# Kernel tuning notes

Hardware: AMD Instinct MI355X
Metric: run time of the kernel (lower is better)

## Reference

```python
import jax, jax.numpy as jnp
import numpy as np

T, B, OBS, H, P, L, A = 512, 128, 512, 256, 128, 4, 4


def _ln(x, scale, bias, eps=1e-6):
    mu = jnp.mean(x, axis=-1, keepdims=True)
    var = jnp.mean((x - mu) ** 2, axis=-1, keepdims=True)
    return (x - mu) * jax.lax.rsqrt(var + eps) * scale + bias


def _binop(qi, qj):
    # S5 reset-aware associative operator: elements (A, b, reset_flag)
    Ai, bi, ci = qi
    Aj, bj, cj = qj
    A = (Aj * Ai) * (1.0 - cj) + Aj * cj
    b = (Aj * bi + bj) * (1.0 - cj) + bj * cj
    c = ci * (1.0 - cj) + cj
    return A, b, c


def _s5_layer(x, dones, h0, scale, bias, lam_re, lam_im, b_re, b_im, c_re, c_im, d_vec, log_step, glu_W, glu_b):
    # x: (T,B,H) real, dones: (T,B), h0: (B,P) complex64
    skip = x
    u = _ln(x, scale, bias)                                  # prenorm
    lam = lam_re + 1j * lam_im                               # (P,)
    step = jnp.exp(log_step)                                 # (P,)
    lam_bar = jnp.exp(lam * step)                            # ZOH discretization
    B_bar = ((lam_bar - 1.0) / lam)[:, None] * (b_re + 1j * b_im)  # (P,H)
    Bu = jnp.einsum('tbh,ph->tbp', u.astype(jnp.complex64), B_bar)  # (T,B,P)
    A_el = jnp.concatenate([jnp.ones((1, B, P), jnp.complex64),
                            jnp.broadcast_to(lam_bar.astype(jnp.complex64), (T, B, P))], axis=0)
    b_el = jnp.concatenate([h0[None], Bu], axis=0)
    c_el = jnp.concatenate([jnp.zeros((1, B, 1), jnp.float32), dones[..., None]], axis=0)
    _, xs, _ = jax.lax.associative_scan(_binop, (A_el, b_el, c_el), axis=0)
    xs = xs[1:]                                              # (T,B,P) complex states
    new_h = xs[-1]
    C = c_re + 1j * c_im                                     # (H,P)
    ys = 2.0 * jnp.real(jnp.einsum('tbp,hp->tbh', xs, C)) + d_vec * u  # conj_sym output + D*u
    z = _ln(ys, scale, bias)                                 # gtrxl norm (shared LayerNorm params)
    z = jax.nn.gelu(z)                                       # half_glu1
    z = z * jax.nn.sigmoid(z @ glu_W + glu_b)
    return skip + z, new_h


def setup_inputs() -> dict:
    key = jax.random.key(0)
    ks = jax.random.split(key, 40)
    f32 = jnp.float32

    def n(i, shape, s=1.0):
        return jax.random.normal(ks[i], shape, f32) * s

    inp = {}
    inp['obs'] = n(0, (T, B, OBS))
    inp['dones'] = (jax.random.uniform(ks[1], (T, B)) < 0.01).astype(f32)
    inp['hidden_re'] = jnp.zeros((L, B, P), f32)
    inp['hidden_im'] = jnp.zeros((L, B, P), f32)
    inp['enc0_W'] = n(2, (OBS, 128), 1.0 / np.sqrt(OBS))
    inp['enc0_b'] = jnp.zeros((128,), f32)
    inp['enc1_W'] = n(3, (128, H), 1.0 / np.sqrt(128))
    inp['enc1_b'] = jnp.zeros((H,), f32)
    inp['norm_scale'] = jnp.ones((L, H), f32)
    inp['norm_bias'] = jnp.zeros((L, H), f32)
    inp['Lambda_re'] = -0.5 * jax.random.uniform(ks[4], (L, P), f32) - 0.1
    inp['Lambda_im'] = n(5, (L, P), np.pi)
    inp['B_re'] = n(6, (L, P, H), 1.0 / np.sqrt(H))
    inp['B_im'] = n(7, (L, P, H), 1.0 / np.sqrt(H))
    inp['C_re'] = n(8, (L, H, P), 1.0 / np.sqrt(2 * P))
    inp['C_im'] = n(9, (L, H, P), 1.0 / np.sqrt(2 * P))
    inp['D'] = n(10, (L, H))
    inp['log_step'] = jax.random.uniform(ks[11], (L, P), f32, np.log(1e-3), np.log(1e-1))
    inp['glu_W'] = n(12, (L, H, H), 1.0 / np.sqrt(H))
    inp['glu_b'] = jnp.zeros((L, H), f32)
    inp['ab0_W'] = n(13, (H, 128), 1.0 / np.sqrt(H))
    inp['ab0_b'] = jnp.zeros((128,), f32)
    inp['ab1_W'] = n(14, (128, 128), 1.0 / np.sqrt(128))
    inp['ab1_b'] = jnp.zeros((128,), f32)
    inp['adec_W'] = n(15, (128, A), 0.01 / np.sqrt(128))
    inp['adec_b'] = jnp.full((A,), 0.5, f32)
    inp['log_std'] = jnp.full((A,), -0.7, f32)
    inp['vb0_W'] = n(16, (H, 128), 1.0 / np.sqrt(H))
    inp['vb0_b'] = jnp.zeros((128,), f32)
    inp['vb1_W'] = n(17, (128, 128), 1.0 / np.sqrt(128))
    inp['vb1_b'] = jnp.zeros((128,), f32)
    inp['vdec_W'] = n(18, (128, 1), 1.0 / np.sqrt(128))
    inp['vdec_b'] = jnp.zeros((1,), f32)
    return inp


def reference(obs, dones, hidden_re, hidden_im, enc0_W, enc0_b, enc1_W, enc1_b,
              norm_scale, norm_bias, Lambda_re, Lambda_im, B_re, B_im, C_re, C_im,
              D, log_step, glu_W, glu_b, ab0_W, ab0_b, ab1_W, ab1_b, adec_W, adec_b,
              log_std, vb0_W, vb0_b, vb1_W, vb1_b, vdec_W, vdec_b):
    e = jax.nn.leaky_relu(obs @ enc0_W + enc0_b)
    e = jax.nn.leaky_relu(e @ enc1_W + enc1_b)
    h0 = (hidden_re + 1j * hidden_im).astype(jnp.complex64)  # (L,B,P)
    new_h = []
    for l in range(L):
        e, hl = _s5_layer(e, dones, h0[l], norm_scale[l], norm_bias[l],
                          Lambda_re[l], Lambda_im[l], B_re[l], B_im[l],
                          C_re[l], C_im[l], D[l], log_step[l], glu_W[l], glu_b[l])
        new_h.append(hl)
    new_h = jnp.stack(new_h)
    am = jax.nn.leaky_relu(e @ ab0_W + ab0_b)
    am = jax.nn.leaky_relu(am @ ab1_W + ab1_b)
    am = am @ adec_W + adec_b                                # actor mean (T,B,A)
    v = jax.nn.leaky_relu(e @ vb0_W + vb0_b)
    v = jax.nn.leaky_relu(v @ vb1_W + vb1_b)
    v = v @ vdec_W + vdec_b                                  # critic (T,B,1)
    sc = jnp.broadcast_to(jnp.exp(log_std), am.shape)        # Normal scale (pi params)
    out = jnp.concatenate([am, sc, v], axis=-1)              # (T,B,2A+1)
    return out, jnp.real(new_h), jnp.imag(new_h)
```

## Files before the change

kernel.cpp:

```cpp
#include <hip/hip_runtime.h>
#include <math.h>

#define TT 512
#define BB 128
#define OBSD 512
#define HD 256
#define PD 128
#define LD 4
#define NTB (TT*BB)

typedef __bf16 bf16x8 __attribute__((ext_vector_type(8)));
typedef float  f32x4  __attribute__((ext_vector_type(4)));

__device__ __forceinline__ float bf2f(unsigned short u) {
    return __uint_as_float(((unsigned)u) << 16);
}
__device__ __forceinline__ unsigned short f2bf(float f) {
    unsigned u = __float_as_uint(f);
    unsigned r = (u + 0x7FFFu + ((u >> 16) & 1u)) >> 16;
    return (unsigned short)r;
}
__device__ __forceinline__ float gelu_f(float x) {
    float x3 = x * x * x;
    return 0.5f * x * (1.f + tanhf(0.7978845608028654f * (x + 0.044715f * x3)));
}

template<int MODE, int NJ>
__global__ __launch_bounds__(512) void mgemm2(
    const unsigned short* __restrict__ A, const unsigned short* __restrict__ BT,
    int K, int LDA, const float* __restrict__ bias,
    const float* __restrict__ lnsc, const float* __restrict__ lnbi,
    const unsigned short* __restrict__ aux1, unsigned short* Xio,
    unsigned short* __restrict__ U, int wU)
{
    constexpr int NJW = NJ / 2;
    constexpr int LPS = 2 + NJW;
    const int N = NJ * 64;
    __shared__ unsigned short smA[3 * 2048];
    __shared__ unsigned short smB[3 * NJ * 2048];
    float2 (*red)[8] = reinterpret_cast<float2(*)[8]>(&smA[0]);
    int tid = threadIdx.x;
    int lane = tid & 63, w = tid >> 6;
    int m16 = lane & 15, quad = lane >> 4;
    int m0 = blockIdx.x * 64;

    f32x4 acc[4][NJW] = {};

    auto stage = [&](int slot, int kt) {
        int k0 = kt << 5;
#pragma unroll
        for (int j = 0; j < 2; ++j) {
            int chunk = w * 2 + j;
            int e = chunk * 128 + lane * 2;
            int row = e >> 5, kb = e & 31;
            const unsigned short* g = A + (size_t)(m0 + row) * LDA + k0 + kb;
            __builtin_amdgcn_global_load_lds(
                (const __attribute__((address_space(1))) void*)g,
                (__attribute__((address_space(3))) void*)(smA + slot * 2048 + chunk * 128 + lane * 2),
                4, 0, 0);
        }
#pragma unroll
        for (int j = 0; j < NJW; ++j) {
            int chunk = w * NJW + j;
            int e = chunk * 512 + lane * 8;
            int p = e >> 11, r = (e >> 5) & 63, kq = e & 31;
            const unsigned short* g = BT + (size_t)(p * 64 + r) * K + k0 + kq;
            __builtin_amdgcn_global_load_lds(
                (const __attribute__((address_space(1))) void*)g,
                (__attribute__((address_space(3))) void*)(smB + slot * NJ * 2048 + chunk * 512 + lane * 8),
                16, 0, 0);
        }
    };

    int nk = K >> 5;
    stage(0, 0);
    stage(1, 1);
    int cur = 0, nxt = 2;
    for (int t = 0; t < nk; ++t) {
        int rem = nk - 1 - t;
        if (rem >= 2) {
            stage(nxt, t + 2);
            nxt = (nxt == 2) ? 0 : nxt + 1;
            asm volatile("s_waitcnt vmcnt(%0)" :: "i"(2 * LPS) : "memory");
        } else if (rem == 1) {
            asm volatile("s_waitcnt vmcnt(%0)" :: "i"(LPS) : "memory");
        } else {
            asm volatile("s_waitcnt vmcnt(0)" ::: "memory");
        }
        __builtin_amdgcn_s_barrier();
        __builtin_amdgcn_sched_barrier(0);
        bf16x8 af[4], bfr[NJW];
#pragma unroll
        for (int mi = 0; mi < 4; ++mi)
            af[mi] = *(const bf16x8*)(smA + cur * 2048 + (mi * 16 + m16) * 32 + quad * 8);
#pragma unroll
        for (int nj = 0; nj < NJW; ++nj)
            bfr[nj] = *(const bf16x8*)(smB + cur * NJ * 2048 + (w * NJW + nj) * 512 + m16 * 32 + quad * 8);
#pragma unroll
        for (int mi = 0; mi < 4; ++mi)
#pragma unroll
            for (int nj = 0; nj < NJW; ++nj)
                acc[mi][nj] = __builtin_amdgcn_mfma_f32_16x16x32_bf16(
                    bfr[nj], af[mi], acc[mi][nj], 0, 0, 0);
        __builtin_amdgcn_sched_barrier(0);
        __builtin_amdgcn_s_barrier();
        cur = (cur == 2) ? 0 : cur + 1;
    }

    int colb = w * (NJW * 16) + quad * 4;

    if (MODE == 1) {
#pragma unroll
        for (int mi = 0; mi < 4; ++mi) {
            size_t rowb = (size_t)(m0 + mi * 16 + m16) * N;
#pragma unroll
            for (int nj = 0; nj < NJW; ++nj) {
                ushort4 o = { f2bf(acc[mi][nj][0]), f2bf(acc[mi][nj][1]),
                              f2bf(acc[mi][nj][2]), f2bf(acc[mi][nj][3]) };
                *(ushort4*)(U + rowb + colb + nj * 16) = o;
            }
        }
        return;
    }

#pragma unroll
    for (int mi = 0; mi < 4; ++mi) {
        size_t rowb = (size_t)(m0 + mi * 16 + m16) * N;
        float s = 0.f, q = 0.f;
#pragma unroll
        for (int nj = 0; nj < NJW; ++nj) {
            float4 bn = *(const float4*)(bias + colb + nj * 16);
            ushort4 a1, xo;
            if (MODE == 2 || MODE == 3) a1 = *(const ushort4*)(aux1 + rowb + colb + nj * 16);
            if (MODE == 3)              xo = *(const ushort4*)(Xio + rowb + colb + nj * 16);
            float vv[4];
#pragma unroll
            for (int r = 0; r < 4; ++r) {
                float v = acc[mi][nj][r];
                float bv = (r == 0) ? bn.x : (r == 1) ? bn.y : (r == 2) ? bn.z : bn.w;
                if (MODE == 0 || MODE == 4) {
                    v += bv; v = v > 0.f ? v : 0.01f * v;
                } else if (MODE == 2) {
                    float u = bf2f(r == 0 ? a1.x : r == 1 ? a1.y : r == 2 ? a1.z : a1.w);
                    v += bv * u;
                } else if (MODE == 3) {
                    float zz = bf2f(r == 0 ? a1.x : r == 1 ? a1.y : r == 2 ? a1.z : a1.w);
                    float xx = bf2f(r == 0 ? xo.x : r == 1 ? xo.y : r == 2 ? xo.z : xo.w);
                    float sg = 1.f / (1.f + expf(-(v + bv)));
                    v = xx + zz * sg;
                }
                vv[r] = v;
                acc[mi][nj][r] = v;
                s += v; q += v * v;
            }
            if (MODE == 0 || MODE == 3) {
                ushort4 o = { f2bf(vv[0]), f2bf(vv[1]), f2bf(vv[2]), f2bf(vv[3]) };
                *(ushort4*)(Xio + rowb + colb + nj * 16) = o;
            } else if (MODE == 4) {
                ushort4 o = { f2bf(vv[0]), f2bf(vv[1]), f2bf(vv[2]), f2bf(vv[3]) };
                *(ushort4*)(U + rowb + colb + nj * 16) = o;
            }
        }
        if (MODE != 4 && (MODE != 3 || wU)) {
            s += __shfl_xor(s, 16); q += __shfl_xor(q, 16);
            s += __shfl_xor(s, 32); q += __shfl_xor(q, 32);
            if (quad == 0) red[mi * 16 + m16][w] = float2{s, q};
        }
    }
    if (MODE == 4 || (MODE == 3 && !wU)) return;
    __syncthreads();

#pragma unroll
    for (int mi = 0; mi < 4; ++mi) {
        int row_l = mi * 16 + m16;
        float S = 0.f, Q = 0.f;
#pragma unroll
        for (int ww = 0; ww < 8; ++ww) {
            float2 tv = red[row_l][ww];
            S += tv.x; Q += tv.y;
        }
        float mu = S * (1.f / 256.f);
        float var = Q * (1.f / 256.f) - mu * mu;
        float rstd = rsqrtf(var + 1e-6f);
        size_t rowb = (size_t)(m0 + row_l) * N;
#pragma unroll
        for (int nj = 0; nj < NJW; ++nj) {
            float4 ls = *(const float4*)(lnsc + colb + nj * 16);
            float4 lb = *(const float4*)(lnbi + colb + nj * 16);
            float o[4];
#pragma unroll
            for (int r = 0; r < 4; ++r) {
                float sc = (r == 0) ? ls.x : (r == 1) ? ls.y : (r == 2) ? ls.z : ls.w;
                float bi = (r == 0) ? lb.x : (r == 1) ? lb.y : (r == 2) ? lb.z : lb.w;
                float v = (acc[mi][nj][r] - mu) * rstd * sc + bi;
                if (MODE == 2) v = gelu_f(v);
                o[r] = v;
            }
            ushort4 ov = { f2bf(o[0]), f2bf(o[1]), f2bf(o[2]), f2bf(o[3]) };
            *(ushort4*)(U + rowb + colb + nj * 16) = ov;
        }
    }
}

__global__ __launch_bounds__(256) void mgemm_obs(
    const float* __restrict__ A, const unsigned short* __restrict__ BT,
    unsigned short* __restrict__ U, const float* __restrict__ bias)
{
    const int K = 512, NJ = 2, N = 128;
    __shared__ unsigned short smA[64 * 32];
    __shared__ unsigned short smB[NJ * 64 * 32];
    int tid = threadIdx.x;
    int lane = tid & 63, w = tid >> 6;
    int m16 = lane & 15, quad = lane >> 4;
    int m0 = blockIdx.x * 64;

    f32x4 acc[4][NJ] = {};
    for (int k0 = 0; k0 < K; k0 += 32) {
#pragma unroll
        for (int p = 0; p < 2; ++p) {
            int idx = p * 256 + tid;
            int r = idx >> 3, kq = (idx & 7) * 4;
            float4 v = *(const float4*)(A + (size_t)(m0 + r) * K + k0 + kq);
            ushort4 o = { f2bf(v.x), f2bf(v.y), f2bf(v.z), f2bf(v.w) };
            *(ushort4*)(smA + r * 32 + kq) = o;
        }
#pragma unroll
        for (int p = 0; p < NJ; ++p) {
            const unsigned short* g = BT + (size_t)(p * 64 + (tid >> 2)) * K + k0 + (tid & 3) * 8;
            unsigned short* l = smB + p * 2048 + tid * 8;
            __builtin_amdgcn_global_load_lds(
                (const __attribute__((address_space(1))) void*)g,
                (__attribute__((address_space(3))) void*)l, 16, 0, 0);
        }
        __syncthreads();
        bf16x8 af[4], bfr[NJ];
#pragma unroll
        for (int mi = 0; mi < 4; ++mi)
            af[mi] = *(const bf16x8*)(smA + (mi * 16 + m16) * 32 + quad * 8);
#pragma unroll
        for (int nj = 0; nj < NJ; ++nj)
            bfr[nj] = *(const bf16x8*)(smB + (w * NJ * 16 + nj * 16 + m16) * 32 + quad * 8);
#pragma unroll
        for (int mi = 0; mi < 4; ++mi)
#pragma unroll
            for (int nj = 0; nj < NJ; ++nj)
                acc[mi][nj] = __builtin_amdgcn_mfma_f32_16x16x32_bf16(
                    bfr[nj], af[mi], acc[mi][nj], 0, 0, 0);
        __syncthreads();
    }
    int colb = w * NJ * 16 + quad * 4;
#pragma unroll
    for (int mi = 0; mi < 4; ++mi) {
        size_t rowb = (size_t)(m0 + mi * 16 + m16) * N;
#pragma unroll
        for (int nj = 0; nj < NJ; ++nj) {
            float4 bv = *(const float4*)(bias + colb + nj * 16);
            float v0 = acc[mi][nj][0] + bv.x; v0 = v0 > 0.f ? v0 : 0.01f * v0;
            float v1 = acc[mi][nj][1] + bv.y; v1 = v1 > 0.f ? v1 : 0.01f * v1;
            float v2 = acc[mi][nj][2] + bv.z; v2 = v2 > 0.f ? v2 : 0.01f * v2;
            float v3 = acc[mi][nj][3] + bv.w; v3 = v3 > 0.f ? v3 : 0.01f * v3;
            ushort4 o = { f2bf(v0), f2bf(v1), f2bf(v2), f2bf(v3) };
            *(ushort4*)(U + rowb + colb + nj * 16) = o;
        }
    }
}

__global__ __launch_bounds__(512) void scan2_k(
    const unsigned short* __restrict__ bu, unsigned short* __restrict__ xs,
    const float* __restrict__ dones,
    const float* __restrict__ h0re, const float* __restrict__ h0im,
    const float* __restrict__ lamre, const float* __restrict__ lamim,
    const float* __restrict__ lstep,
    float* __restrict__ outre, float* __restrict__ outim)
{
    __shared__ float sdone[TT];
    __shared__ float4 ssum[8][64];
    __shared__ float2 shin[8][64];
    int tid = threadIdx.x;
    int b  = blockIdx.x >> 1;
    int ph = blockIdx.x & 1;
    int chunk = tid >> 6, pl = tid & 63;
    int p = ph * 64 + pl;
    sdone[tid] = dones[tid * BB + b];
    float lr = lamre[p], li = lamim[p];
    float st = expf(lstep[p]);
    float er = expf(lr * st);
    float ar = er * cosf(li * st);
    float ai = er * sinf(li * st);
    __syncthreads();

    int t0 = chunk * 64;
    unsigned buf[64];
    float Ar = 1.f, Ai = 0.f, br = 0.f, bi = 0.f;
#pragma unroll
    for (int j = 0; j < 64; ++j) {
        size_t off = ((size_t)(t0 + j) * BB + b) * 256 + 2 * p;
        unsigned v = *(const unsigned*)(bu + off);
        buf[j] = v;
        float bur = bf2f((unsigned short)(v & 0xFFFFu));
        float bui = bf2f((unsigned short)(v >> 16));
        if (sdone[t0 + j] != 0.f) {
            Ar = 0.f; Ai = 0.f; br = bur; bi = bui;
        } else {
            float nAr = ar * Ar - ai * Ai;
            float nAi = ar * Ai + ai * Ar;
            float nbr = fmaf(ar, br, fmaf(-ai, bi, bur));
            float nbi = fmaf(ar, bi, fmaf(ai, br, bui));
            Ar = nAr; Ai = nAi; br = nbr; bi = nbi;
        }
    }
    ssum[chunk][pl] = float4{Ar, Ai, br, bi};
    __syncthreads();
    if (tid < 64) {
        int gid = b * 128 + p;
        float hr = h0re[gid], hi = h0im[gid];
#pragma unroll
        for (int c = 0; c < 8; ++c) {
            shin[c][pl] = float2{hr, hi};
            float4 s = ssum[c][pl];
            float nhr = fmaf(s.x, hr, fmaf(-s.y, hi, s.z));
            float nhi = fmaf(s.x, hi, fmaf(s.y, hr, s.w));
            hr = nhr; hi = nhi;
        }
        outre[gid] = hr; outim[gid] = hi;
    }
    __syncthreads();
    float hr = shin[chunk][pl].x, hi = shin[chunk][pl].y;
#pragma unroll
    for (int j = 0; j < 64; ++j) {
        unsigned v = buf[j];
        float bur = bf2f((unsigned short)(v & 0xFFFFu));
        float bui = bf2f((unsigned short)(v >> 16));
        float nr, ni;
        if (sdone[t0 + j] != 0.f) { nr = bur; ni = bui; }
        else {
            nr = fmaf(ar, hr, fmaf(-ai, hi, bur));
            ni = fmaf(ar, hi, fmaf(ai, hr, bui));
        }
        hr = nr; hi = ni;
        size_t off = ((size_t)(t0 + j) * BB + b) * 256 + 2 * p;
        *(unsigned*)(xs + off) = ((unsigned)f2bf(ni) << 16) | f2bf(nr);
    }
}

__global__ __launch_bounds__(256) void prep_k(
    const float* __restrict__ Br, const float* __restrict__ Bi,
    const float* __restrict__ Cr, const float* __restrict__ Ci,
    const float* __restrict__ Lr, const float* __restrict__ Li,
    const float* __restrict__ ls, unsigned short* bbarT, unsigned short* ccatT)
{
    int gid = blockIdx.x * 256 + threadIdx.x;
    int l = gid >> 15;
    int rem = gid & 32767;
    int p = rem >> 8;
    int h = rem & 255;
    float lr = Lr[l * PD + p], li = Li[l * PD + p];
    float st = expf(ls[l * PD + p]);
    float er = expf(lr * st);
    float lbr = er * cosf(li * st);
    float lbi = er * sinf(li * st);
    float nr = lbr - 1.f, ni = lbi;
    float den = lr * lr + li * li;
    float fr = (nr * lr + ni * li) / den;
    float fi = (ni * lr - nr * li) / den;
    float bre = Br[(size_t)(l * PD + p) * HD + h];
    float bim = Bi[(size_t)(l * PD + p) * HD + h];
    size_t lb = (size_t)l * 65536;
    bbarT[lb + (size_t)(2 * p) * 256 + h]     = f2bf(fr * bre - fi * bim);
    bbarT[lb + (size_t)(2 * p + 1) * 256 + h] = f2bf(fr * bim + fi * bre);
    float cre = Cr[(size_t)(l * HD + h) * PD + p];
    float cim = Ci[(size_t)(l * HD + h) * PD + p];
    ccatT[lb + (size_t)h * 256 + 2 * p]     = f2bf(2.f * cre);
    ccatT[lb + (size_t)h * 256 + 2 * p + 1] = f2bf(-2.f * cim);
}

__global__ __launch_bounds__(256) void tcvt_k(const float* __restrict__ in,
    unsigned short* __restrict__ out, int K, int N)
{
    int gid = blockIdx.x * 256 + threadIdx.x;
    if (gid >= K * N) return;
    int k = gid / N, n = gid - k * N;
    out[(size_t)n * K + k] = f2bf(in[gid]);
}

__global__ __launch_bounds__(256) void tcvt4_k(const float* __restrict__ in,
    unsigned short* __restrict__ out)
{
    int gid = blockIdx.x * 256 + threadIdx.x;
    int l = gid >> 16;
    int rem = gid & 65535;
    int k = rem >> 8, n = rem & 255;
    out[(size_t)l * 65536 + (size_t)n * 256 + k] = f2bf(in[gid]);
}

__global__ __launch_bounds__(256) void catb_k(const float* __restrict__ a,
    const float* __restrict__ b, float* __restrict__ out)
{
    int i = threadIdx.x;
    out[i] = (i < 128) ? a[i] : b[i - 128];
}

__global__ __launch_bounds__(256) void head_k(
    const unsigned short* __restrict__ am2, const unsigned short* __restrict__ v2,
    const float* __restrict__ adW, const float* __restrict__ adb,
    const float* __restrict__ lstd,
    const float* __restrict__ vdW, const float* __restrict__ vdb,
    float* out)
{
    int wid = threadIdx.x >> 6, lane = threadIdx.x & 63;
    size_t row = (size_t)blockIdx.x * 4 + wid;
    float a1 = bf2f(am2[row * 128 + lane]);
    float a2 = bf2f(am2[row * 128 + 64 + lane]);
    float w1 = bf2f(v2[row * 128 + lane]);
    float w2 = bf2f(v2[row * 128 + 64 + lane]);
    float vals[5];
#pragma unroll
    for (int a = 0; a < 4; ++a)
        vals[a] = a1 * adW[lane * 4 + a] + a2 * adW[(lane + 64) * 4 + a];
    vals[4] = w1 * vdW[lane] + w2 * vdW[64 + lane];
#pragma unroll
    for (int off = 32; off; off >>= 1)
#pragma unroll
        for (int k = 0; k < 5; ++k) vals[k] += __shfl_xor(vals[k], off);
    if (lane == 0) {
        size_t o = row * 9;
#pragma unroll
        for (int a = 0; a < 4; ++a) out[o + a] = vals[a] + adb[a];
#pragma unroll
        for (int a = 0; a < 4; ++a) out[o + 4 + a] = expf(lstd[a]);
        out[o + 8] = vals[4] + vdb[0];
    }
}

extern "C" void kernel_launch(void* const* d_in, const int* in_sizes, int n_in,
                              void* d_out, int out_size, void* d_ws, size_t ws_size,
                              hipStream_t stream) {
    (void)in_sizes; (void)n_in; (void)out_size; (void)ws_size;
    const float* obs     = (const float*)d_in[0];
    const float* dones   = (const float*)d_in[1];
    const float* hre     = (const float*)d_in[2];
    const float* him     = (const float*)d_in[3];
    const float* enc0_W  = (const float*)d_in[4];
    const float* enc0_b  = (const float*)d_in[5];
    const float* enc1_W  = (const float*)d_in[6];
    const float* enc1_b  = (const float*)d_in[7];
    const float* nsc     = (const float*)d_in[8];
    const float* nbi     = (const float*)d_in[9];
    const float* Lre     = (const float*)d_in[10];
    const float* Lim     = (const float*)d_in[11];
    const float* B_re    = (const float*)d_in[12];
    const float* B_im    = (const float*)d_in[13];
    const float* C_re    = (const float*)d_in[14];
    const float* C_im    = (const float*)d_in[15];
    const float* Dv      = (const float*)d_in[16];
    const float* lstep   = (const float*)d_in[17];
    const float* glu_W   = (const float*)d_in[18];
    const float* glu_b   = (const float*)d_in[19];
    const float* ab0_W   = (const float*)d_in[20];
    const float* ab0_b   = (const float*)d_in[21];
    const float* ab1_W   = (const float*)d_in[22];
    const float* ab1_b   = (const float*)d_in[23];
    const float* adec_W  = (const float*)d_in[24];
    const float* adec_b  = (const float*)d_in[25];
    const float* log_std = (const float*)d_in[26];
    const float* vb0_W   = (const float*)d_in[27];
    const float* vb0_b   = (const float*)d_in[28];
    const float* vb1_W   = (const float*)d_in[29];
    const float* vb1_b   = (const float*)d_in[30];
    const float* vdec_W  = (const float*)d_in[31];
    const float* vdec_b  = (const float*)d_in[32];

    const size_t MB = (size_t)1 << 20;
    char* wsb = (char*)d_ws;
    unsigned short* XS    = (unsigned short*)(wsb);
    unsigned short* AMV1  = (unsigned short*)(wsb);
    unsigned short* AM2   = (unsigned short*)(wsb + 32 * MB);
    unsigned short* V2    = (unsigned short*)(wsb + 48 * MB);
    unsigned short* U1    = (unsigned short*)(wsb + 64 * MB);
    unsigned short* X     = (unsigned short*)(wsb + 96 * MB);
    unsigned short* U     = (unsigned short*)(wsb + 128 * MB);
    unsigned short* BU    = (unsigned short*)(wsb + 160 * MB);
    char* wgt = wsb + 192 * MB;
    unsigned short* BBART = (unsigned short*)(wgt);
    unsigned short* CCATT = (unsigned short*)(wgt + 512 * 1024);
    unsigned short* GLUT  = (unsigned short*)(wgt + 1024 * 1024);
    unsigned short* E0T   = (unsigned short*)(wgt + 1536 * 1024);
    unsigned short* E1T   = (unsigned short*)(wgt + 1664 * 1024);
    unsigned short* AB0VT = (unsigned short*)(wgt + 1728 * 1024);
    unsigned short* AB1T  = (unsigned short*)(wgt + 1856 * 1024);
    unsigned short* VB1T  = (unsigned short*)(wgt + 1888 * 1024);
    float*          CB0   = (float*)(wgt + 1920 * 1024);

    float* out   = (float*)d_out;
    float* outre = out + (size_t)NTB * 9;
    float* outim = outre + LD * BB * PD;

    prep_k<<<512, 256, 0, stream>>>(B_re, B_im, C_re, C_im, Lre, Lim, lstep, BBART, CCATT);
    tcvt_k<<<256, 256, 0, stream>>>(enc0_W, E0T, 512, 128);
    tcvt_k<<<128, 256, 0, stream>>>(enc1_W, E1T, 128, 256);
    tcvt4_k<<<1024, 256, 0, stream>>>(glu_W, GLUT);
    tcvt_k<<<128, 256, 0, stream>>>(ab0_W, AB0VT, 256, 128);
    tcvt_k<<<128, 256, 0, stream>>>(vb0_W, AB0VT + 128 * 256, 256, 128);
    tcvt_k<<<64, 256, 0, stream>>>(ab1_W, AB1T, 128, 128);
    tcvt_k<<<64, 256, 0, stream>>>(vb1_W, VB1T, 128, 128);
    catb_k<<<1, 256, 0, stream>>>(ab0_b, vb0_b, CB0);

    mgemm_obs<<<1024, 256, 0, stream>>>(obs, E0T, U1, enc0_b);
    mgemm2<0, 4><<<1024, 512, 0, stream>>>(U1, E1T, 128, 128, enc1_b, nsc, nbi, nullptr, X, U, 1);

    for (int l = 0; l < LD; ++l) {
        mgemm2<1, 4><<<1024, 512, 0, stream>>>(U, BBART + (size_t)l * 65536, 256, 256,
                                               nullptr, nullptr, nullptr, nullptr, nullptr, BU, 0);
        scan2_k<<<256, 512, 0, stream>>>(BU, XS, dones, hre + l * BB * PD, him + l * BB * PD,
                                         Lre + l * PD, Lim + l * PD, lstep + l * PD,
                                         outre + l * BB * PD, outim + l * BB * PD);
        mgemm2<2, 4><<<1024, 512, 0, stream>>>(XS, CCATT + (size_t)l * 65536, 256, 256,
                                               Dv + l * HD, nsc + l * HD, nbi + l * HD, U, nullptr, U, 1);
        const float* nsc2 = nsc + ((l + 1 < LD) ? (l + 1) * HD : 0);
        const float* nbi2 = nbi + ((l + 1 < LD) ? (l + 1) * HD : 0);
        mgemm2<3, 4><<<1024, 512, 0, stream>>>(U, GLUT + (size_t)l * 65536, 256, 256,
                                               glu_b + l * HD, nsc2, nbi2, U, X, U, (l + 1 < LD) ? 1 : 0);
    }

    mgemm2<4, 4><<<1024, 512, 0, stream>>>(X, AB0VT, 256, 256, CB0, nullptr, nullptr, nullptr, nullptr, AMV1, 0);
    mgemm2<4, 2><<<1024, 512, 0, stream>>>(AMV1, AB1T, 128, 256, ab1_b, nullptr, nullptr, nullptr, nullptr, AM2, 0);
    mgemm2<4, 2><<<1024, 512, 0, stream>>>(AMV1 + 128, VB1T, 128, 256, vb1_b, nullptr, nullptr, nullptr, nullptr, V2, 0);
    head_k<<<NTB / 4, 256, 0, stream>>>(AM2, V2, adec_W, adec_b, log_std, vdec_W, vdec_b, out);
}
```

Before: 960.5 us.

## Fuse GLU with next-layer B projection and fuse MLP heads into one kernel

Adds glu_bu_k, which runs the GLU GEMM, residual and next-layer LayerNorm, then keeps the normalized row tile in shared memory and runs the next layer's B_bar projection without a round trip through global memory. Adds head_fused_k, which chains the actor and critic MLP layers and the decoder dot products in one kernel, replacing three GEMMs and head_k. It also makes K a compile-time template parameter and splits the scan into four P-groups per batch with 16 time chunks to raise parallelism. The cost is more shared memory per block, which may lower occupancy, and the fused kernels use double buffering where the old GEMM used three stages.

```diff
diff --git a/kernel.cpp b/kernel.cpp
--- a/kernel.cpp
+++ b/kernel.cpp
@@ -25,16 +25,17 @@
     return 0.5f * x * (1.f + tanhf(0.7978845608028654f * (x + 0.044715f * x3)));
 }
 
-template<int MODE, int NJ>
+template<int MODE, int NJ, int NK>
 __global__ __launch_bounds__(512) void mgemm2(
     const unsigned short* __restrict__ A, const unsigned short* __restrict__ BT,
-    int K, int LDA, const float* __restrict__ bias,
+    int LDA, const float* __restrict__ bias,
     const float* __restrict__ lnsc, const float* __restrict__ lnbi,
     const unsigned short* __restrict__ aux1, unsigned short* Xio,
     unsigned short* __restrict__ U, int wU)
 {
     constexpr int NJW = NJ / 2;
     constexpr int LPS = 2 + NJW;
+    constexpr int K = NK * 32;
     const int N = NJ * 64;
     __shared__ unsigned short smA[3 * 2048];
     __shared__ unsigned short smB[3 * NJ * 2048];
@@ -56,8 +57,7 @@
             const unsigned short* g = A + (size_t)(m0 + row) * LDA + k0 + kb;
             __builtin_amdgcn_global_load_lds(
                 (const __attribute__((address_space(1))) void*)g,
-                (__attribute__((address_space(3))) void*)(smA + slot * 2048 + chunk * 128 + lane * 2),
-                4, 0, 0);
+                (__attribute__((address_space(3))) void*)(smA + slot * 2048 + e), 4, 0, 0);
         }
 #pragma unroll
         for (int j = 0; j < NJW; ++j) {
@@ -67,12 +67,11 @@
             const unsigned short* g = BT + (size_t)(p * 64 + r) * K + k0 + kq;
             __builtin_amdgcn_global_load_lds(
                 (const __attribute__((address_space(1))) void*)g,
-                (__attribute__((address_space(3))) void*)(smB + slot * NJ * 2048 + chunk * 512 + lane * 8),
-                16, 0, 0);
+                (__attribute__((address_space(3))) void*)(smB + slot * NJ * 2048 + e), 16, 0, 0);
         }
     };
 
-    int nk = K >> 5;
+    int nk = NK;
     stage(0, 0);
     stage(1, 1);
     int cur = 0, nxt = 2;
@@ -138,7 +137,7 @@
             for (int r = 0; r < 4; ++r) {
                 float v = acc[mi][nj][r];
                 float bv = (r == 0) ? bn.x : (r == 1) ? bn.y : (r == 2) ? bn.z : bn.w;
-                if (MODE == 0 || MODE == 4) {
+                if (MODE == 0) {
                     v += bv; v = v > 0.f ? v : 0.01f * v;
                 } else if (MODE == 2) {
                     float u = bf2f(r == 0 ? a1.x : r == 1 ? a1.y : r == 2 ? a1.z : a1.w);
@@ -156,18 +155,15 @@
             if (MODE == 0 || MODE == 3) {
                 ushort4 o = { f2bf(vv[0]), f2bf(vv[1]), f2bf(vv[2]), f2bf(vv[3]) };
                 *(ushort4*)(Xio + rowb + colb + nj * 16) = o;
-            } else if (MODE == 4) {
-                ushort4 o = { f2bf(vv[0]), f2bf(vv[1]), f2bf(vv[2]), f2bf(vv[3]) };
-                *(ushort4*)(U + rowb + colb + nj * 16) = o;
             }
         }
-        if (MODE != 4 && (MODE != 3 || wU)) {
+        if (MODE != 3 || wU) {
             s += __shfl_xor(s, 16); q += __shfl_xor(q, 16);
             s += __shfl_xor(s, 32); q += __shfl_xor(q, 32);
             if (quad == 0) red[mi * 16 + m16][w] = float2{s, q};
         }
     }
-    if (MODE == 4 || (MODE == 3 && !wU)) return;
+    if (MODE == 3 && !wU) return;
     __syncthreads();
 
 #pragma unroll
@@ -199,6 +195,377 @@
             ushort4 ov = { f2bf(o[0]), f2bf(o[1]), f2bf(o[2]), f2bf(o[3]) };
             *(ushort4*)(U + rowb + colb + nj * 16) = ov;
         }
+    }
+}
+
+__global__ __launch_bounds__(512) void glu_bu_k(
+    const unsigned short* __restrict__ Z,
+    const unsigned short* __restrict__ GT,
+    const unsigned short* __restrict__ BT2,
+    const float* __restrict__ glub,
+    const float* __restrict__ ns2, const float* __restrict__ nb2,
+    unsigned short* __restrict__ Xio,
+    unsigned short* __restrict__ Uo,
+    unsigned short* __restrict__ BUo)
+{
+    const int N = 256;
+    __shared__ unsigned short smA[2 * 2048];
+    __shared__ unsigned short smB[2 * 8192];
+    __shared__ unsigned short zbuf[64 * 264];
+    float2 (*red)[8] = reinterpret_cast<float2(*)[8]>(&smA[0]);
+    int tid = threadIdx.x;
+    int lane = tid & 63, w = tid >> 6;
+    int m16 = lane & 15, quad = lane >> 4;
+    int m0 = blockIdx.x * 64;
+    int colb = w * 32 + quad * 4;
+
+    f32x4 acc[4][2] = {};
+
+    auto stage1 = [&](int slot, int kt) {
+        int k0 = kt << 5;
+#pragma unroll
+        for (int j = 0; j < 2; ++j) {
+            int e = (w * 2 + j) * 128 + lane * 2;
+            int row = e >> 5, kb = e & 31;
+            const unsigned short* g = Z + (size_t)(m0 + row) * 256 + k0 + kb;
+            __builtin_amdgcn_global_load_lds(
+                (const __attribute__((address_space(1))) void*)g,
+                (__attribute__((address_space(3))) void*)(smA + slot * 2048 + e), 4, 0, 0);
+        }
+#pragma unroll
+        for (int j = 0; j < 2; ++j) {
+            int e = (w * 2 + j) * 512 + lane * 8;
+            int p = e >> 11, r = (e >> 5) & 63, kq = e & 31;
+            const unsigned short* g = GT + (size_t)(p * 64 + r) * 256 + k0 + kq;
+            __builtin_amdgcn_global_load_lds(
+                (const __attribute__((address_space(1))) void*)g,
+                (__attribute__((address_space(3))) void*)(smB + slot * 8192 + e), 16, 0, 0);
+        }
+    };
+    auto stage2 = [&](int slot, int kt) {
+        int k0 = kt << 5;
+#pragma unroll
+        for (int j = 0; j < 2; ++j) {
+            int e = (w * 2 + j) * 512 + lane * 8;
+            int p = e >> 11, r = (e >> 5) & 63, kq = e & 31;
+            const unsigned short* g = BT2 + (size_t)(p * 64 + r) * 256 + k0 + kq;
+            __builtin_amdgcn_global_load_lds(
+                (const __attribute__((address_space(1))) void*)g,
+                (__attribute__((address_space(3))) void*)(smB + slot * 8192 + e), 16, 0, 0);
+        }
+    };
+
+    stage1(0, 0);
+    for (int t = 0; t < 8; ++t) {
+        int cur = t & 1;
+        if (t + 1 < 8) {
+            stage1(cur ^ 1, t + 1);
+            asm volatile("s_waitcnt vmcnt(4)" ::: "memory");
+        } else {
+            asm volatile("s_waitcnt vmcnt(0)" ::: "memory");
+        }
+        __builtin_amdgcn_s_barrier();
+        __builtin_amdgcn_sched_barrier(0);
+        bf16x8 af[4], bfr[2];
+#pragma unroll
+        for (int mi = 0; mi < 4; ++mi)
+            af[mi] = *(const bf16x8*)(smA + cur * 2048 + (mi * 16 + m16) * 32 + quad * 8);
+#pragma unroll
+        for (int nj = 0; nj < 2; ++nj)
+            bfr[nj] = *(const bf16x8*)(smB + cur * 8192 + (w * 2 + nj) * 512 + m16 * 32 + quad * 8);
+#pragma unroll
+        for (int mi = 0; mi < 4; ++mi)
+#pragma unroll
+            for (int nj = 0; nj < 2; ++nj)
+                acc[mi][nj] = __builtin_amdgcn_mfma_f32_16x16x32_bf16(
+                    bfr[nj], af[mi], acc[mi][nj], 0, 0, 0);
+        __builtin_amdgcn_sched_barrier(0);
+        __builtin_amdgcn_s_barrier();
+    }
+
+    stage2(0, 0);
+
+#pragma unroll
+    for (int mi = 0; mi < 4; ++mi) {
+        int row_l = mi * 16 + m16;
+        size_t rowb = (size_t)(m0 + row_l) * N;
+        float s = 0.f, q = 0.f;
+#pragma unroll
+        for (int nj = 0; nj < 2; ++nj) {
+            float4 gb = *(const float4*)(glub + colb + nj * 16);
+            ushort4 a1 = *(const ushort4*)(Z + rowb + colb + nj * 16);
+            ushort4 xo = *(const ushort4*)(Xio + rowb + colb + nj * 16);
+            float vv[4];
+#pragma unroll
+            for (int r = 0; r < 4; ++r) {
+                float v = acc[mi][nj][r];
+                float bv = (r == 0) ? gb.x : (r == 1) ? gb.y : (r == 2) ? gb.z : gb.w;
+                float zz = bf2f(r == 0 ? a1.x : r == 1 ? a1.y : r == 2 ? a1.z : a1.w);
+                float xx = bf2f(r == 0 ? xo.x : r == 1 ? xo.y : r == 2 ? xo.z : xo.w);
+                float sg = 1.f / (1.f + expf(-(v + bv)));
+                v = xx + zz * sg;
+                vv[r] = v;
+                acc[mi][nj][r] = v;
+                s += v; q += v * v;
+            }
+            ushort4 o = { f2bf(vv[0]), f2bf(vv[1]), f2bf(vv[2]), f2bf(vv[3]) };
+            *(ushort4*)(Xio + rowb + colb + nj * 16) = o;
+        }
+        s += __shfl_xor(s, 16); q += __shfl_xor(q, 16);
+        s += __shfl_xor(s, 32); q += __shfl_xor(q, 32);
+        if (quad == 0) red[row_l][w] = float2{s, q};
+    }
+    __syncthreads();
+
+#pragma unroll
+    for (int mi = 0; mi < 4; ++mi) {
+        int row_l = mi * 16 + m16;
+        float S = 0.f, Q = 0.f;
+#pragma unroll
+        for (int ww = 0; ww < 8; ++ww) { float2 tv = red[row_l][ww]; S += tv.x; Q += tv.y; }
+        float mu = S * (1.f / 256.f);
+        float var = Q * (1.f / 256.f) - mu * mu;
+        float rstd = rsqrtf(var + 1e-6f);
+        size_t rowb = (size_t)(m0 + row_l) * N;
+#pragma unroll
+        for (int nj = 0; nj < 2; ++nj) {
+            float4 ls = *(const float4*)(ns2 + colb + nj * 16);
+            float4 lb = *(const float4*)(nb2 + colb + nj * 16);
+            float o[4];
+#pragma unroll
+            for (int r = 0; r < 4; ++r) {
+                float sc = (r == 0) ? ls.x : (r == 1) ? ls.y : (r == 2) ? ls.z : ls.w;
+                float bi = (r == 0) ? lb.x : (r == 1) ? lb.y : (r == 2) ? lb.z : lb.w;
+                o[r] = (acc[mi][nj][r] - mu) * rstd * sc + bi;
+            }
+            ushort4 ov = { f2bf(o[0]), f2bf(o[1]), f2bf(o[2]), f2bf(o[3]) };
+            *(ushort4*)(Uo + rowb + colb + nj * 16) = ov;
+            *(ushort4*)(zbuf + row_l * 264 + colb + nj * 16) = ov;
+        }
+    }
+    __syncthreads();
+
+    f32x4 acc2[4][2] = {};
+    for (int t = 0; t < 8; ++t) {
+        int cur = t & 1;
+        if (t + 1 < 8) {
+            stage2(cur ^ 1, t + 1);
+            asm volatile("s_waitcnt vmcnt(2)" ::: "memory");
+        } else {
+            asm volatile("s_waitcnt vmcnt(0)" ::: "memory");
+        }
+        __builtin_amdgcn_s_barrier();
+        __builtin_amdgcn_sched_barrier(0);
+        bf16x8 af[4], bfr[2];
+#pragma unroll
+        for (int mi = 0; mi < 4; ++mi)
+            af[mi] = *(const bf16x8*)(zbuf + (mi * 16 + m16) * 264 + t * 32 + quad * 8);
+#pragma unroll
+        for (int nj = 0; nj < 2; ++nj)
+            bfr[nj] = *(const bf16x8*)(smB + cur * 8192 + (w * 2 + nj) * 512 + m16 * 32 + quad * 8);
+#pragma unroll
+        for (int mi = 0; mi < 4; ++mi)
+#pragma unroll
+            for (int nj = 0; nj < 2; ++nj)
+                acc2[mi][nj] = __builtin_amdgcn_mfma_f32_16x16x32_bf16(
+                    bfr[nj], af[mi], acc2[mi][nj], 0, 0, 0);
+        __builtin_amdgcn_sched_barrier(0);
+        __builtin_amdgcn_s_barrier();
+    }
+#pragma unroll
+    for (int mi = 0; mi < 4; ++mi) {
+        size_t rowb = (size_t)(m0 + mi * 16 + m16) * N;
+#pragma unroll
+        for (int nj = 0; nj < 2; ++nj) {
+            ushort4 o = { f2bf(acc2[mi][nj][0]), f2bf(acc2[mi][nj][1]),
+                          f2bf(acc2[mi][nj][2]), f2bf(acc2[mi][nj][3]) };
+            *(ushort4*)(BUo + rowb + colb + nj * 16) = o;
+        }
+    }
+}
+
+__global__ __launch_bounds__(512) void head_fused_k(
+    const unsigned short* __restrict__ Xp, const unsigned short* __restrict__ W0T,
+    const float* __restrict__ cb0,
+    const unsigned short* __restrict__ AB1T, const unsigned short* __restrict__ VB1T,
+    const float* __restrict__ ab1b, const float* __restrict__ vb1b,
+    const float* __restrict__ adW, const float* __restrict__ adb,
+    const float* __restrict__ lstd,
+    const float* __restrict__ vdW, const float* __restrict__ vdb,
+    float* __restrict__ out)
+{
+    __shared__ unsigned short smA[2 * 2048];
+    __shared__ unsigned short smB[2 * 8192];
+    __shared__ unsigned short zbuf[64 * 264];
+    float (*redh)[8][4] = reinterpret_cast<float(*)[8][4]>(&smA[0]);
+    int tid = threadIdx.x;
+    int lane = tid & 63, w = tid >> 6;
+    int m16 = lane & 15, quad = lane >> 4;
+    int m0 = blockIdx.x * 64;
+    int colb = w * 32 + quad * 4;
+
+    f32x4 acc[4][2] = {};
+
+    auto stage1 = [&](int slot, int kt) {
+        int k0 = kt << 5;
+#pragma unroll
+        for (int j = 0; j < 2; ++j) {
+            int e = (w * 2 + j) * 128 + lane * 2;
+            int row = e >> 5, kb = e & 31;
+            const unsigned short* g = Xp + (size_t)(m0 + row) * 256 + k0 + kb;
+            __builtin_amdgcn_global_load_lds(
+                (const __attribute__((address_space(1))) void*)g,
+                (__attribute__((address_space(3))) void*)(smA + slot * 2048 + e), 4, 0, 0);
+        }
+#pragma unroll
+        for (int j = 0; j < 2; ++j) {
+            int e = (w * 2 + j) * 512 + lane * 8;
+            int p = e >> 11, r = (e >> 5) & 63, kq = e & 31;
+            const unsigned short* g = W0T + (size_t)(p * 64 + r) * 256 + k0 + kq;
+            __builtin_amdgcn_global_load_lds(
+                (const __attribute__((address_space(1))) void*)g,
+                (__attribute__((address_space(3))) void*)(smB + slot * 8192 + e), 16, 0, 0);
+        }
+    };
+    auto stage2 = [&](int slot, int kt) {
+        int k0 = kt << 5;
+#pragma unroll
+        for (int j = 0; j < 2; ++j) {
+            int e = (w * 2 + j) * 512 + lane * 8;
+            int r = e >> 5, kq = e & 31;
+            const unsigned short* g = (r < 128)
+                ? AB1T + (size_t)r * 128 + k0 + kq
+                : VB1T + (size_t)(r - 128) * 128 + k0 + kq;
+            __builtin_amdgcn_global_load_lds(
+                (const __attribute__((address_space(1))) void*)g,
+                (__attribute__((address_space(3))) void*)(smB + slot * 8192 + e), 16, 0, 0);
+        }
+    };
+
+    stage1(0, 0);
+    for (int t = 0; t < 8; ++t) {
+        int cur = t & 1;
+        if (t + 1 < 8) {
+            stage1(cur ^ 1, t + 1);
+            asm volatile("s_waitcnt vmcnt(4)" ::: "memory");
+        } else {
+            asm volatile("s_waitcnt vmcnt(0)" ::: "memory");
+        }
+        __builtin_amdgcn_s_barrier();
+        __builtin_amdgcn_sched_barrier(0);
+        bf16x8 af[4], bfr[2];
+#pragma unroll
+        for (int mi = 0; mi < 4; ++mi)
+            af[mi] = *(const bf16x8*)(smA + cur * 2048 + (mi * 16 + m16) * 32 + quad * 8);
+#pragma unroll
+        for (int nj = 0; nj < 2; ++nj)
+            bfr[nj] = *(const bf16x8*)(smB + cur * 8192 + (w * 2 + nj) * 512 + m16 * 32 + quad * 8);
+#pragma unroll
+        for (int mi = 0; mi < 4; ++mi)
+#pragma unroll
+            for (int nj = 0; nj < 2; ++nj)
+                acc[mi][nj] = __builtin_amdgcn_mfma_f32_16x16x32_bf16(
+                    bfr[nj], af[mi], acc[mi][nj], 0, 0, 0);
+        __builtin_amdgcn_sched_barrier(0);
+        __builtin_amdgcn_s_barrier();
+    }
+    stage2(0, 0);
+#pragma unroll
+    for (int mi = 0; mi < 4; ++mi) {
+        int row_l = mi * 16 + m16;
+#pragma unroll
+        for (int nj = 0; nj < 2; ++nj) {
+            float4 bn = *(const float4*)(cb0 + colb + nj * 16);
+            float v0 = acc[mi][nj][0] + bn.x; v0 = v0 > 0.f ? v0 : 0.01f * v0;
+            float v1 = acc[mi][nj][1] + bn.y; v1 = v1 > 0.f ? v1 : 0.01f * v1;
+            float v2 = acc[mi][nj][2] + bn.z; v2 = v2 > 0.f ? v2 : 0.01f * v2;
+            float v3 = acc[mi][nj][3] + bn.w; v3 = v3 > 0.f ? v3 : 0.01f * v3;
+            ushort4 o = { f2bf(v0), f2bf(v1), f2bf(v2), f2bf(v3) };
+            *(ushort4*)(zbuf + row_l * 264 + colb + nj * 16) = o;
+        }
+    }
+    __syncthreads();
+
+    f32x4 acc2[4][2] = {};
+    int abase = (w < 4) ? 0 : 128;
+    for (int t = 0; t < 4; ++t) {
+        int cur = t & 1;
+        if (t + 1 < 4) {
+            stage2(cur ^ 1, t + 1);
+            asm volatile("s_waitcnt vmcnt(2)" ::: "memory");
+        } else {
+            asm volatile("s_waitcnt vmcnt(0)" ::: "memory");
+        }
+        __builtin_amdgcn_s_barrier();
+        __builtin_amdgcn_sched_barrier(0);
+        bf16x8 af[4], bfr[2];
+#pragma unroll
+        for (int mi = 0; mi < 4; ++mi)
+            af[mi] = *(const bf16x8*)(zbuf + (mi * 16 + m16) * 264 + abase + t * 32 + quad * 8);
+#pragma unroll
+        for (int nj = 0; nj < 2; ++nj) {
+            int rb = abase + (w & 3) * 32 + nj * 16 + m16;
+            bfr[nj] = *(const bf16x8*)(smB + cur * 8192 + rb * 32 + quad * 8);
+        }
+#pragma unroll
+        for (int mi = 0; mi < 4; ++mi)
+#pragma unroll
+            for (int nj = 0; nj < 2; ++nj)
+                acc2[mi][nj] = __builtin_amdgcn_mfma_f32_16x16x32_bf16(
+                    bfr[nj], af[mi], acc2[mi][nj], 0, 0, 0);
+        __builtin_amdgcn_sched_barrier(0);
+        __builtin_amdgcn_s_barrier();
+    }
+
+    float pd[4][4] = {};
+    float pv[4] = {0.f, 0.f, 0.f, 0.f};
+#pragma unroll
+    for (int nj = 0; nj < 2; ++nj)
+#pragma unroll
+        for (int r = 0; r < 4; ++r) {
+            int c = (w & 3) * 32 + nj * 16 + quad * 4 + r;
+            float bb = (w < 4) ? ab1b[c] : vb1b[c];
+            float4 aw = {0.f, 0.f, 0.f, 0.f};
+            float vw = 0.f;
+            if (w < 4) aw = *(const float4*)(adW + c * 4);
+            else       vw = vdW[c];
+#pragma unroll
+            for (int mi = 0; mi < 4; ++mi) {
+                float v = acc2[mi][nj][r] + bb;
+                v = v > 0.f ? v : 0.01f * v;
+                if (w < 4) {
+                    pd[mi][0] += v * aw.x; pd[mi][1] += v * aw.y;
+                    pd[mi][2] += v * aw.z; pd[mi][3] += v * aw.w;
+                } else {
+                    pv[mi] += v * vw;
+                }
+            }
+        }
+#pragma unroll
+    for (int mi = 0; mi < 4; ++mi) {
+        int row_l = mi * 16 + m16;
+        if (w < 4) {
+#pragma unroll
+            for (int a = 0; a < 4; ++a) {
+                float x = pd[mi][a];
+                x += __shfl_xor(x, 16); x += __shfl_xor(x, 32);
+                if (quad == 0) redh[row_l][w][a] = x;
+            }
+        } else {
+            float x = pv[mi];
+            x += __shfl_xor(x, 16); x += __shfl_xor(x, 32);
+            if (quad == 0) redh[row_l][w][0] = x;
+        }
+    }
+    __syncthreads();
+    if (tid < 64) {
+        size_t o = (size_t)(m0 + tid) * 9;
+#pragma unroll
+        for (int a = 0; a < 4; ++a)
+            out[o + a] = redh[tid][0][a] + redh[tid][1][a] + redh[tid][2][a] + redh[tid][3][a] + adb[a];
+#pragma unroll
+        for (int a = 0; a < 4; ++a) out[o + 4 + a] = expf(lstd[a]);
+        out[o + 8] = redh[tid][4][0] + redh[tid][5][0] + redh[tid][6][0] + redh[tid][7][0] + vdb[0];
     }
 }
 
@@ -274,13 +641,13 @@
     float* __restrict__ outre, float* __restrict__ outim)
 {
     __shared__ float sdone[TT];
-    __shared__ float4 ssum[8][64];
-    __shared__ float2 shin[8][64];
+    __shared__ float4 ssum[16][32];
+    __shared__ float2 shin[16][32];
     int tid = threadIdx.x;
-    int b  = blockIdx.x >> 1;
-    int ph = blockIdx.x & 1;
-    int chunk = tid >> 6, pl = tid & 63;
-    int p = ph * 64 + pl;
+    int b  = blockIdx.x >> 2;
+    int ph = blockIdx.x & 3;
+    int chunk = tid >> 5, pl = tid & 31;
+    int p = ph * 32 + pl;
     sdone[tid] = dones[tid * BB + b];
     float lr = lamre[p], li = lamim[p];
     float st = expf(lstep[p]);
@@ -289,11 +656,11 @@
     float ai = er * sinf(li * st);
     __syncthreads();
 
-    int t0 = chunk * 64;
-    unsigned buf[64];
+    int t0 = chunk * 32;
+    unsigned buf[32];
     float Ar = 1.f, Ai = 0.f, br = 0.f, bi = 0.f;
 #pragma unroll
-    for (int j = 0; j < 64; ++j) {
+    for (int j = 0; j < 32; ++j) {
         size_t off = ((size_t)(t0 + j) * BB + b) * 256 + 2 * p;
         unsigned v = *(const unsigned*)(bu + off);
         buf[j] = v;
@@ -311,13 +678,13 @@
     }
     ssum[chunk][pl] = float4{Ar, Ai, br, bi};
     __syncthreads();
-    if (tid < 64) {
-        int gid = b * 128 + p;
+    if (tid < 32) {
+        int gid = b * 128 + ph * 32 + tid;
         float hr = h0re[gid], hi = h0im[gid];
 #pragma unroll
-        for (int c = 0; c < 8; ++c) {
-            shin[c][pl] = float2{hr, hi};
-            float4 s = ssum[c][pl];
+        for (int c = 0; c < 16; ++c) {
+            shin[c][tid] = float2{hr, hi};
+            float4 s = ssum[c][tid];
             float nhr = fmaf(s.x, hr, fmaf(-s.y, hi, s.z));
             float nhi = fmaf(s.x, hi, fmaf(s.y, hr, s.w));
             hr = nhr; hi = nhi;
@@ -327,7 +694,7 @@
     __syncthreads();
     float hr = shin[chunk][pl].x, hi = shin[chunk][pl].y;
 #pragma unroll
-    for (int j = 0; j < 64; ++j) {
+    for (int j = 0; j < 32; ++j) {
         unsigned v = buf[j];
         float bur = bf2f((unsigned short)(v & 0xFFFFu));
         float bui = bf2f((unsigned short)(v >> 16));
@@ -398,38 +765,6 @@
 {
     int i = threadIdx.x;
     out[i] = (i < 128) ? a[i] : b[i - 128];
-}
-
-__global__ __launch_bounds__(256) void head_k(
-    const unsigned short* __restrict__ am2, const unsigned short* __restrict__ v2,
-    const float* __restrict__ adW, const float* __restrict__ adb,
-    const float* __restrict__ lstd,
-    const float* __restrict__ vdW, const float* __restrict__ vdb,
-    float* out)
-{
-    int wid = threadIdx.x >> 6, lane = threadIdx.x & 63;
-    size_t row = (size_t)blockIdx.x * 4 + wid;
-    float a1 = bf2f(am2[row * 128 + lane]);
-    float a2 = bf2f(am2[row * 128 + 64 + lane]);
-    float w1 = bf2f(v2[row * 128 + lane]);
-    float w2 = bf2f(v2[row * 128 + 64 + lane]);
-    float vals[5];
-#pragma unroll
-    for (int a = 0; a < 4; ++a)
-        vals[a] = a1 * adW[lane * 4 + a] + a2 * adW[(lane + 64) * 4 + a];
-    vals[4] = w1 * vdW[lane] + w2 * vdW[64 + lane];
-#pragma unroll
-    for (int off = 32; off; off >>= 1)
-#pragma unroll
-        for (int k = 0; k < 5; ++k) vals[k] += __shfl_xor(vals[k], off);
-    if (lane == 0) {
-        size_t o = row * 9;
-#pragma unroll
-        for (int a = 0; a < 4; ++a) out[o + a] = vals[a] + adb[a];
-#pragma unroll
-        for (int a = 0; a < 4; ++a) out[o + 4 + a] = expf(lstd[a]);
-        out[o + 8] = vals[4] + vdb[0];
-    }
 }
 
 extern "C" void kernel_launch(void* const* d_in, const int* in_sizes, int n_in,
@@ -473,9 +808,6 @@
     const size_t MB = (size_t)1 << 20;
     char* wsb = (char*)d_ws;
     unsigned short* XS    = (unsigned short*)(wsb);
-    unsigned short* AMV1  = (unsigned short*)(wsb);
-    unsigned short* AM2   = (unsigned short*)(wsb + 32 * MB);
-    unsigned short* V2    = (unsigned short*)(wsb + 48 * MB);
     unsigned short* U1    = (unsigned short*)(wsb + 64 * MB);
     unsigned short* X     = (unsigned short*)(wsb + 96 * MB);
     unsigned short* U     = (unsigned short*)(wsb + 128 * MB);
@@ -506,24 +838,28 @@
     catb_k<<<1, 256, 0, stream>>>(ab0_b, vb0_b, CB0);
 
     mgemm_obs<<<1024, 256, 0, stream>>>(obs, E0T, U1, enc0_b);
-    mgemm2<0, 4><<<1024, 512, 0, stream>>>(U1, E1T, 128, 128, enc1_b, nsc, nbi, nullptr, X, U, 1);
-
+    mgemm2<0, 4, 4><<<1024, 512, 0, stream>>>(U1, E1T, 128, enc1_b, nsc, nbi, nullptr, X, U, 1);
+
+    mgemm2<1, 4, 8><<<1024, 512, 0, stream>>>(U, BBART, 256,
+                                           nullptr, nullptr, nullptr, nullptr, nullptr, BU, 0);
     for (int l = 0; l < LD; ++l) {
-        mgemm2<1, 4><<<1024, 512, 0, stream>>>(U, BBART + (size_t)l * 65536, 256, 256,
-                                               nullptr, nullptr, nullptr, nullptr, nullptr, BU, 0);
-        scan2_k<<<256, 512, 0, stream>>>(BU, XS, dones, hre + l * BB * PD, him + l * BB * PD,
+        scan2_k<<<512, 512, 0, stream>>>(BU, XS, dones, hre + l * BB * PD, him + l * BB * PD,
                                          Lre + l * PD, Lim + l * PD, lstep + l * PD,
                                          outre + l * BB * PD, outim + l * BB * PD);
-        mgemm2<2, 4><<<1024, 512, 0, stream>>>(XS, CCATT + (size_t)l * 65536, 256, 256,
+        mgemm2<2, 4, 8><<<1024, 512, 0, stream>>>(XS, CCATT + (size_t)l * 65536, 256,
                                                Dv + l * HD, nsc + l * HD, nbi + l * HD, U, nullptr, U, 1);
-        const float* nsc2 = nsc + ((l + 1 < LD) ? (l + 1) * HD : 0);
-        const float* nbi2 = nbi + ((l + 1 < LD) ? (l + 1) * HD : 0);
-        mgemm2<3, 4><<<1024, 512, 0, stream>>>(U, GLUT + (size_t)l * 65536, 256, 256,
-                                               glu_b + l * HD, nsc2, nbi2, U, X, U, (l + 1 < LD) ? 1 : 0);
-    }
-
-    mgemm2<4, 4><<<1024, 512, 0, stream>>>(X, AB0VT, 256, 256, CB0, nullptr, nullptr, nullptr, nullptr, AMV1, 0);
-    mgemm2<4, 2><<<1024, 512, 0, stream>>>(AMV1, AB1T, 128, 256, ab1_b, nullptr, nullptr, nullptr, nullptr, AM2, 0);
-    mgemm2<4, 2><<<1024, 512, 0, stream>>>(AMV1 + 128, VB1T, 128, 256, vb1_b, nullptr, nullptr, nullptr, nullptr, V2, 0);
-    head_k<<<NTB / 4, 256, 0, stream>>>(AM2, V2, adec_W, adec_b, log_std, vdec_W, vdec_b, out);
-}
+        if (l + 1 < LD) {
+            glu_bu_k<<<1024, 512, 0, stream>>>(U, GLUT + (size_t)l * 65536,
+                                               BBART + (size_t)(l + 1) * 65536,
+                                               glu_b + l * HD,
+                                               nsc + (l + 1) * HD, nbi + (l + 1) * HD,
+                                               X, U, BU);
+        } else {
+            mgemm2<3, 4, 8><<<1024, 512, 0, stream>>>(U, GLUT + (size_t)l * 65536, 256,
+                                               glu_b + l * HD, nsc, nbi, U, X, U, 0);
+        }
+    }
+
+    head_fused_k<<<1024, 512, 0, stream>>>(X, AB0VT, CB0, AB1T, VB1T, ab1_b, vb1_b,
+                                           adec_W, adec_b, log_std, vdec_W, vdec_b, out);
+}
```

After: 872.4 us. 1.1x faster.
